# Kernel tuning notes

Hardware: AMD Instinct MI355X
Metric: run time of the kernel (lower is better)

The kernel has to match this reference:

```python
import jax, jax.numpy as jnp
import numpy as np

N_NODES = 50000
N_EDGES = 800000
C_IN = 128
C_OUT = 128


def setup_inputs() -> dict:
    key = jax.random.key(0)
    k1, k2, k3, k4 = jax.random.split(key, 4)
    x = jax.random.normal(k1, (N_NODES, C_IN), dtype=jnp.float32)
    edge_index = jax.random.randint(k2, (2, N_EDGES), 0, N_NODES, dtype=jnp.int64)
    # Linear(in, out): weight [out, in], bias [out]
    W = jax.random.normal(k3, (C_OUT, C_IN), dtype=jnp.float32) * (1.0 / np.sqrt(C_IN))
    b = jax.random.normal(k4, (C_OUT,), dtype=jnp.float32) * 0.01
    return {"x": x, "edge_index": edge_index, "W": W, "b": b}


def reference(x, edge_index, W, b):
    # GCN layer: out = D^{-1/2} (A + I) D^{-1/2} x W^T + b
    # Implemented as sparse gather/segment-sum (same math as the dense
    # adjacency matmul in the original, without the O(N^2) blowup).
    n = x.shape[0]
    loops = jnp.arange(n, dtype=edge_index.dtype)
    row = jnp.concatenate([edge_index[0], loops])  # [E+N]
    col = jnp.concatenate([edge_index[1], loops])  # [E+N]
    # degree over col index (as in pyg_utils.degree(edge_index[1], ...))
    ones = jnp.ones(row.shape[0], dtype=x.dtype)
    deg = jax.ops.segment_sum(ones, col, num_segments=n)
    deg_inv_sqrt = jnp.where(deg > 0, jax.lax.rsqrt(deg), 0.0).astype(x.dtype)
    norm = deg_inv_sqrt[row] * deg_inv_sqrt[col]  # [E+N]
    # aggregate: out[i] = sum_{(i,j) in edges} norm * x[j]
    msgs = x[col] * norm[:, None]  # [E+N, C_in]
    agg = jax.ops.segment_sum(msgs, row, num_segments=n)  # [N, C_in]
    return agg @ W.T + b
```

## Files before the change

### kernel.cpp

```cpp
#include <hip/hip_runtime.h>
#include <hip/hip_bf16.h>
#include <hip/hip_fp16.h>

#define C 128
#define NCH 32768
#define CN 2
#define CNODES (CN * NCH)
#define BE 64

typedef _Float16 f16x8 __attribute__((ext_vector_type(8)));
typedef _Float16 f16x4 __attribute__((ext_vector_type(4)));
typedef float f32x4 __attribute__((ext_vector_type(4)));

__global__ __launch_bounds__(256) void k_hist(
        const int* __restrict__ row, const int* __restrict__ col,
        unsigned char* __restrict__ part_row, unsigned char* __restrict__ part_col,
        unsigned char* __restrict__ tag, int E) {
    __shared__ unsigned lh[NCH / 4];
    int bid = blockIdx.x;
    int side = (bid >= CN * BE) ? 1 : 0;
    int lb = side ? bid - CN * BE : bid;
    int c = lb >> 6;
    int b = lb & (BE - 1);
    int tid = threadIdx.x;
    for (int i = tid * 4; i < NCH / 4; i += 1024) {
        lh[i] = 0u; lh[i + 1] = 0u; lh[i + 2] = 0u; lh[i + 3] = 0u;
    }
    __syncthreads();
    int EPB = (E + BE - 1) / BE;
    int base = b * EPB;
    int end = min(base + EPB, E);
    const int* src = side ? col : row;

#define PROC_ROW(rv, ev)                                                  \
    if (((unsigned)(rv) >> 15) == (unsigned)c) {                          \
        int loc = (rv) & (NCH - 1);                                       \
        unsigned sh = ((unsigned)loc & 3u) << 3;                          \
        unsigned old = atomicAdd(&lh[loc >> 2], 1u << sh);                \
        tag[ev] = (unsigned char)((old >> sh) & 0xffu);                   \
    }
#define PROC_COL(rv)                                                      \
    if (((unsigned)(rv) >> 15) == (unsigned)c) {                          \
        int loc = (rv) & (NCH - 1);                                       \
        atomicAdd(&lh[loc >> 2], 1u << (((unsigned)loc & 3u) << 3));      \
    }
    int nv = 0;
    if ((((uintptr_t)(src + base)) & 15) == 0) nv = (end - base) >> 2;
    const int4* src4 = (const int4*)(src + base);
    if (!side) {
        for (int it = tid; it < nv; it += 256) {
            int4 v = src4[it];
            int e0 = base + it * 4;
            PROC_ROW(v.x, e0);
            PROC_ROW(v.y, e0 + 1);
            PROC_ROW(v.z, e0 + 2);
            PROC_ROW(v.w, e0 + 3);
        }
        for (int e = base + nv * 4 + tid; e < end; e += 256) {
            int r = src[e];
            PROC_ROW(r, e);
        }
    } else {
        for (int it = tid; it < nv; it += 256) {
            int4 v = src4[it];
            PROC_COL(v.x);
            PROC_COL(v.y);
            PROC_COL(v.z);
            PROC_COL(v.w);
        }
        for (int e = base + nv * 4 + tid; e < end; e += 256) {
            int r = src[e];
            PROC_COL(r);
        }
    }
#undef PROC_ROW
#undef PROC_COL
    __syncthreads();
    unsigned* dst = (unsigned*)((side ? part_col : part_row) + (size_t)b * CNODES + c * NCH);
    for (int i = tid; i < NCH / 4; i += 256) dst[i] = lh[i];
}

__global__ __launch_bounds__(256) void k_reduce_scan(
        unsigned char* __restrict__ part_row, const unsigned char* __restrict__ part_col,
        unsigned* __restrict__ start, unsigned* __restrict__ bsum,
        float* __restrict__ dis, int n) {
    __shared__ unsigned s[256];
    int t = threadIdx.x;
    int i = blockIdx.x * 256 + t;
    unsigned acc = 0;
    if (i < n) {
#pragma unroll 8
        for (int b = 0; b < BE; ++b) {
            size_t off = (size_t)b * CNODES + i;
            unsigned v = part_row[off];
            part_row[off] = (unsigned char)acc;
            acc += v;
        }
        unsigned d = 0;
#pragma unroll 8
        for (int b = 0; b < BE; ++b) d += part_col[(size_t)b * CNODES + i];
        dis[i] = rsqrtf((float)(d + 1u));
    }
    unsigned v = acc;
    s[t] = v;
    __syncthreads();
    for (int off = 1; off < 256; off <<= 1) {
        unsigned add = (t >= off) ? s[t - off] : 0u;
        __syncthreads();
        s[t] += add;
        __syncthreads();
    }
    if (i < n) start[i] = s[t] - v;
    if (t == 255) bsum[blockIdx.x] = s[t];
}

__global__ __launch_bounds__(256) void k_scan_final(unsigned* __restrict__ start,
                                                    const unsigned* __restrict__ bsum,
                                                    int n, int E) {
    __shared__ unsigned s[256];
    int t = threadIdx.x;
    int bid = blockIdx.x;
    s[t] = (t < bid) ? bsum[t] : 0u;
    __syncthreads();
    for (int off = 128; off > 0; off >>= 1) {
        if (t < off) s[t] += s[t + off];
        __syncthreads();
    }
    unsigned base = s[0];
    int i = bid * 256 + t;
    if (i < n) start[i] += base;
    if (i == n) start[i] = (unsigned)E;
}

__global__ __launch_bounds__(256) void k_scatter_gemm(
        const int* __restrict__ row, const int* __restrict__ col,
        const unsigned char* __restrict__ tag, const unsigned char* __restrict__ boff,
        const unsigned* __restrict__ start, int* __restrict__ scol, int E, int SB,
        const float* __restrict__ A, const float* __restrict__ W,
        const float* __restrict__ dis, __half* __restrict__ Z16, int n) {
    __shared__ char lds[128 * 256];
    int bid = blockIdx.x;
    int tid = threadIdx.x;
    if (bid < SB) {
        int e = bid * 256 + tid;
        if (e < E) {
            int EPB = (E + BE - 1) / BE;
            unsigned b = (unsigned)e / (unsigned)EPB;
            int r = row[e];
            unsigned p = start[r] + boff[(size_t)b * CNODES + r] + tag[e];
            scol[p] = col[e];
        }
        return;
    }
    int w = tid >> 6, lane = tid & 63;
    int m0 = (bid - SB) * 128;

#pragma unroll
    for (int i = 0; i < 16; ++i) {
        int fidx = i * 256 + tid;
        int nr = fidx >> 5;
        int c4 = fidx & 31;
        float4 wv = *(const float4*)(W + (size_t)nr * C + c4 * 4);
        f16x4 hh = {(_Float16)wv.x, (_Float16)wv.y, (_Float16)wv.z, (_Float16)wv.w};
        unsigned byte = (unsigned)(nr * 256 + c4 * 8);
        byte ^= (unsigned)((nr & 7) << 4);
        *(f16x4*)(lds + byte) = hh;
    }
    __syncthreads();

    int rbase = m0 + w * 32;
    int q = lane >> 4, rl = lane & 15;
    float dm[2];
#pragma unroll
    for (int mt = 0; mt < 2; ++mt) {
        int r = rbase + mt * 16 + rl;
        dm[mt] = (r < n) ? dis[r] : 0.f;
    }
    f32x4 acc[2][8] = {};
#pragma unroll
    for (int kc = 0; kc < 4; ++kc) {
        f16x8 af[2];
#pragma unroll
        for (int mt = 0; mt < 2; ++mt) {
            int r = rbase + mt * 16 + rl;
            float4 x0 = make_float4(0.f, 0.f, 0.f, 0.f), x1 = x0;
            if (r < n) {
                const float* srcx = A + (size_t)r * C + kc * 32 + q * 8;
                x0 = *(const float4*)srcx;
                x1 = *(const float4*)(srcx + 4);
            }
            float s = dm[mt];
            af[mt][0] = (_Float16)(x0.x * s);
            af[mt][1] = (_Float16)(x0.y * s);
            af[mt][2] = (_Float16)(x0.z * s);
            af[mt][3] = (_Float16)(x0.w * s);
            af[mt][4] = (_Float16)(x1.x * s);
            af[mt][5] = (_Float16)(x1.y * s);
            af[mt][6] = (_Float16)(x1.z * s);
            af[mt][7] = (_Float16)(x1.w * s);
        }
#pragma unroll
        for (int nt = 0; nt < 8; ++nt) {
            int nrow = nt * 16 + rl;
            unsigned byte = (unsigned)(nrow * 256 + kc * 64 + q * 16);
            byte ^= (unsigned)((nrow & 7) << 4);
            f16x8 bf = *(f16x8*)(lds + byte);
            acc[0][nt] = __builtin_amdgcn_mfma_f32_16x16x32_f16(af[0], bf, acc[0][nt], 0, 0, 0);
            acc[1][nt] = __builtin_amdgcn_mfma_f32_16x16x32_f16(af[1], bf, acc[1][nt], 0, 0, 0);
        }
    }
    __syncthreads();

#pragma unroll
    for (int mt = 0; mt < 2; ++mt)
#pragma unroll
        for (int nt = 0; nt < 8; ++nt)
#pragma unroll
            for (int i = 0; i < 4; ++i) {
                int row_l = w * 32 + mt * 16 + q * 4 + i;
                int colh = nt * 16 + rl;
                unsigned byte = (unsigned)(row_l * 256 + colh * 2);
                byte ^= (unsigned)((row_l & 7) << 4);
                *(_Float16*)(lds + byte) = (_Float16)acc[mt][nt][i];
            }
    __syncthreads();

#pragma unroll
    for (int it = 0; it < 8; ++it) {
        int idx = it * 256 + tid;
        int row_l = idx >> 4, c8 = idx & 15;
        unsigned byte = (unsigned)(row_l * 256 + c8 * 16);
        byte ^= (unsigned)((row_l & 7) << 4);
        uint4 v = *(uint4*)(lds + byte);
        int gr = m0 + row_l;
        if (gr < n) *(uint4*)(Z16 + (size_t)gr * C + c8 * 8) = v;
    }
}

__device__ __forceinline__ void add8(uint4 v, float2& a0, float2& a1,
                                     float2& a2, float2& a3) {
    float2 f;
    f = __half22float2(*(__half2*)&v.x); a0.x += f.x; a0.y += f.y;
    f = __half22float2(*(__half2*)&v.y); a1.x += f.x; a1.y += f.y;
    f = __half22float2(*(__half2*)&v.z); a2.x += f.x; a2.y += f.y;
    f = __half22float2(*(__half2*)&v.w); a3.x += f.x; a3.y += f.y;
}

__global__ __launch_bounds__(256) void k_agg(const __half* __restrict__ Z16,
                                             const int* __restrict__ scol,
                                             const unsigned* __restrict__ start,
                                             const float* __restrict__ dis,
                                             const float* __restrict__ bias,
                                             float* __restrict__ out, int n) {
    int wid = threadIdx.x >> 6;
    int lane = threadIdx.x & 63;
    int slot = lane >> 4;
    int g = lane & 15;
    int r = blockIdx.x * 4 + wid;
    if (r >= n) return;
    unsigned s0 = start[r], s1 = start[r + 1];
    float dr = dis[r];
    const uint4* Z4 = (const uint4*)Z16;
    float2 a0 = {0.f, 0.f}, a1 = a0, a2 = a0, a3 = a0;
    if (slot == 0) {
        uint4 v = Z4[(size_t)r * 16 + g];
        add8(v, a0, a1, a2, a3);
    }
    unsigned k = s0;
    for (; k + 16 <= s1; k += 16) {
        int c0 = scol[k + slot];
        int c1 = scol[k + 4 + slot];
        int c2 = scol[k + 8 + slot];
        int c3 = scol[k + 12 + slot];
        uint4 v0 = Z4[(size_t)c0 * 16 + g];
        uint4 v1 = Z4[(size_t)c1 * 16 + g];
        uint4 v2 = Z4[(size_t)c2 * 16 + g];
        uint4 v3 = Z4[(size_t)c3 * 16 + g];
        add8(v0, a0, a1, a2, a3);
        add8(v1, a0, a1, a2, a3);
        add8(v2, a0, a1, a2, a3);
        add8(v3, a0, a1, a2, a3);
    }
    for (; k < s1; k += 4) {
        unsigned ke = k + slot;
        if (ke < s1) {
            int c = scol[ke];
            uint4 v = Z4[(size_t)c * 16 + g];
            add8(v, a0, a1, a2, a3);
        }
    }
    a0.x += __shfl_xor(a0.x, 16); a0.y += __shfl_xor(a0.y, 16);
    a1.x += __shfl_xor(a1.x, 16); a1.y += __shfl_xor(a1.y, 16);
    a2.x += __shfl_xor(a2.x, 16); a2.y += __shfl_xor(a2.y, 16);
    a3.x += __shfl_xor(a3.x, 16); a3.y += __shfl_xor(a3.y, 16);
    a0.x += __shfl_xor(a0.x, 32); a0.y += __shfl_xor(a0.y, 32);
    a1.x += __shfl_xor(a1.x, 32); a1.y += __shfl_xor(a1.y, 32);
    a2.x += __shfl_xor(a2.x, 32); a2.y += __shfl_xor(a2.y, 32);
    a3.x += __shfl_xor(a3.x, 32); a3.y += __shfl_xor(a3.y, 32);
    if (slot == 0) {
        float4 b0 = *(const float4*)(bias + g * 8);
        float4 b1 = *(const float4*)(bias + g * 8 + 4);
        float4 o0, o1;
        o0.x = b0.x + dr * a0.x; o0.y = b0.y + dr * a0.y;
        o0.z = b0.z + dr * a1.x; o0.w = b0.w + dr * a1.y;
        o1.x = b1.x + dr * a2.x; o1.y = b1.y + dr * a2.y;
        o1.z = b1.z + dr * a3.x; o1.w = b1.w + dr * a3.y;
        float* op = out + (size_t)r * C + g * 8;
        *(float4*)op = o0;
        *(float4*)(op + 4) = o1;
    }
}

extern "C" void kernel_launch(void* const* d_in, const int* in_sizes, int n_in,
                              void* d_out, int out_size, void* d_ws, size_t ws_size,
                              hipStream_t stream) {
    const float* x  = (const float*)d_in[0];
    const int*   ei = (const int*)d_in[1];
    const float* W  = (const float*)d_in[2];
    const float* b  = (const float*)d_in[3];
    float* out = (float*)d_out;

    int n = in_sizes[0] / C;
    int E = in_sizes[1] / 2;
    const int* row = ei;
    const int* col = ei + E;

    char* p = (char*)d_ws;
    size_t sz_part = (((size_t)BE * CNODES) + 511) & ~(size_t)511;
    size_t sz_n    = (((size_t)n * 4) + 511) & ~(size_t)511;
    size_t sz_n1   = (((size_t)(n + 1) * 4) + 511) & ~(size_t)511;
    size_t sz_E1   = (((size_t)E) + 511) & ~(size_t)511;
    size_t sz_E4   = (((size_t)E * 4) + 511) & ~(size_t)511;
    size_t off = 0;
    unsigned char*  part_row = (unsigned char*)(p + off);  off += sz_part;
    unsigned char*  part_col = (unsigned char*)(p + off);  off += sz_part;
    unsigned*       start    = (unsigned*)(p + off);       off += sz_n1;
    float*          dis      = (float*)(p + off);          off += sz_n;
    unsigned*       bsum     = (unsigned*)(p + off);       off += 4096;
    unsigned char*  tag      = (unsigned char*)(p + off);  off += sz_E1;
    int*            scol     = (int*)(p + off);            off += sz_E4;
    __half*         z16      = (__half*)(p + off);

    int NT = 256;
    int NB = (n + NT - 1) / NT;
    int SB = (E + NT - 1) / NT;
    int GB = (n + 127) / 128;

    k_hist<<<2 * CN * BE, NT, 0, stream>>>(row, col, part_row, part_col, tag, E);
    k_reduce_scan<<<NB, NT, 0, stream>>>(part_row, part_col, start, bsum, dis, n);
    k_scan_final<<<NB, NT, 0, stream>>>(start, bsum, n, E);
    k_scatter_gemm<<<SB + GB, NT, 0, stream>>>(row, col, tag, part_row, start, scol,
                                               E, SB, x, W, dis, z16, n);
    k_agg<<<(n + 3) / 4, NT, 0, stream>>>(z16, scol, start, dis, b, out, n);
}
```

Baseline: 81.23 us.

## Run GEMM alongside histogram kernel and apply degree scaling afterwards

The dense x·W^T GEMM moves out of the scatter kernel and into the histogram kernel, so it runs concurrently with the edge histogram. Because degrees are not known yet at that point, the D^{-1/2} row scaling is dropped from the GEMM and applied later in a separate elementwise pass over the fp16 result, fused into the scatter kernel. The edge-block count BE doubles to 128 and EPB is rounded to a multiple of 4 so the int4 loads stay aligned. The cost is an extra read and write of the fp16 Z matrix, plus an additional fp16 rounding step.

```diff
diff --git a/kernel.cpp b/kernel.cpp
--- a/kernel.cpp
+++ b/kernel.cpp
@@ -6,31 +6,36 @@
 #define NCH 32768
 #define CN 2
 #define CNODES (CN * NCH)
-#define BE 64
+#define BE 128
 
 typedef _Float16 f16x8 __attribute__((ext_vector_type(8)));
 typedef _Float16 f16x4 __attribute__((ext_vector_type(4)));
 typedef float f32x4 __attribute__((ext_vector_type(4)));
 
-__global__ __launch_bounds__(256) void k_hist(
+__global__ __launch_bounds__(256) void k_hist_gemm(
         const int* __restrict__ row, const int* __restrict__ col,
         unsigned char* __restrict__ part_row, unsigned char* __restrict__ part_col,
-        unsigned char* __restrict__ tag, int E) {
-    __shared__ unsigned lh[NCH / 4];
+        unsigned char* __restrict__ tag, int E, int EPB, int GB,
+        const float* __restrict__ A, const float* __restrict__ W,
+        __half* __restrict__ Y16, int n) {
+    __shared__ char lds[128 * 256];
     int bid = blockIdx.x;
-    int side = (bid >= CN * BE) ? 1 : 0;
-    int lb = side ? bid - CN * BE : bid;
-    int c = lb >> 6;
-    int b = lb & (BE - 1);
     int tid = threadIdx.x;
-    for (int i = tid * 4; i < NCH / 4; i += 1024) {
-        lh[i] = 0u; lh[i + 1] = 0u; lh[i + 2] = 0u; lh[i + 3] = 0u;
-    }
-    __syncthreads();
-    int EPB = (E + BE - 1) / BE;
-    int base = b * EPB;
-    int end = min(base + EPB, E);
-    const int* src = side ? col : row;
+
+    if (bid >= GB) {
+        unsigned* lh = (unsigned*)lds;
+        int lb = bid - GB;
+        int side = (lb >= CN * BE) ? 1 : 0;
+        if (side) lb -= CN * BE;
+        int c = lb >> 7;
+        int b = lb & (BE - 1);
+        for (int i = tid * 4; i < NCH / 4; i += 1024) {
+            lh[i] = 0u; lh[i + 1] = 0u; lh[i + 2] = 0u; lh[i + 3] = 0u;
+        }
+        __syncthreads();
+        int base = b * EPB;
+        int end = min(base + EPB, E);
+        const int* src = side ? col : row;
 
 #define PROC_ROW(rv, ev)                                                  \
     if (((unsigned)(rv) >> 15) == (unsigned)c) {                          \
@@ -44,40 +49,118 @@
         int loc = (rv) & (NCH - 1);                                       \
         atomicAdd(&lh[loc >> 2], 1u << (((unsigned)loc & 3u) << 3));      \
     }
-    int nv = 0;
-    if ((((uintptr_t)(src + base)) & 15) == 0) nv = (end - base) >> 2;
-    const int4* src4 = (const int4*)(src + base);
-    if (!side) {
-        for (int it = tid; it < nv; it += 256) {
-            int4 v = src4[it];
-            int e0 = base + it * 4;
-            PROC_ROW(v.x, e0);
-            PROC_ROW(v.y, e0 + 1);
-            PROC_ROW(v.z, e0 + 2);
-            PROC_ROW(v.w, e0 + 3);
-        }
-        for (int e = base + nv * 4 + tid; e < end; e += 256) {
-            int r = src[e];
-            PROC_ROW(r, e);
-        }
-    } else {
-        for (int it = tid; it < nv; it += 256) {
-            int4 v = src4[it];
-            PROC_COL(v.x);
-            PROC_COL(v.y);
-            PROC_COL(v.z);
-            PROC_COL(v.w);
-        }
-        for (int e = base + nv * 4 + tid; e < end; e += 256) {
-            int r = src[e];
-            PROC_COL(r);
-        }
-    }
+        int nv = (end > base) ? ((end - base) >> 2) : 0;
+        const int4* src4 = (const int4*)(src + base);
+        if (!side) {
+            for (int it = tid; it < nv; it += 256) {
+                int4 v = src4[it];
+                int e0 = base + it * 4;
+                PROC_ROW(v.x, e0);
+                PROC_ROW(v.y, e0 + 1);
+                PROC_ROW(v.z, e0 + 2);
+                PROC_ROW(v.w, e0 + 3);
+            }
+            for (int e = base + nv * 4 + tid; e < end; e += 256) {
+                int r = src[e];
+                PROC_ROW(r, e);
+            }
+        } else {
+            for (int it = tid; it < nv; it += 256) {
+                int4 v = src4[it];
+                PROC_COL(v.x);
+                PROC_COL(v.y);
+                PROC_COL(v.z);
+                PROC_COL(v.w);
+            }
+            for (int e = base + nv * 4 + tid; e < end; e += 256) {
+                int r = src[e];
+                PROC_COL(r);
+            }
+        }
 #undef PROC_ROW
 #undef PROC_COL
-    __syncthreads();
-    unsigned* dst = (unsigned*)((side ? part_col : part_row) + (size_t)b * CNODES + c * NCH);
-    for (int i = tid; i < NCH / 4; i += 256) dst[i] = lh[i];
+        __syncthreads();
+        unsigned* dst = (unsigned*)((side ? part_col : part_row) + (size_t)b * CNODES + c * NCH);
+        for (int i = tid; i < NCH / 4; i += 256) dst[i] = lh[i];
+        return;
+    }
+
+    int w = tid >> 6, lane = tid & 63;
+    int m0 = bid * 128;
+
+#pragma unroll
+    for (int i = 0; i < 16; ++i) {
+        int fidx = i * 256 + tid;
+        int nr = fidx >> 5;
+        int c4 = fidx & 31;
+        float4 wv = *(const float4*)(W + (size_t)nr * C + c4 * 4);
+        f16x4 hh = {(_Float16)wv.x, (_Float16)wv.y, (_Float16)wv.z, (_Float16)wv.w};
+        unsigned byte = (unsigned)(nr * 256 + c4 * 8);
+        byte ^= (unsigned)((nr & 7) << 4);
+        *(f16x4*)(lds + byte) = hh;
+    }
+    __syncthreads();
+
+    int rbase = m0 + w * 32;
+    int q = lane >> 4, rl = lane & 15;
+    f32x4 acc[2][8] = {};
+#pragma unroll
+    for (int kc = 0; kc < 4; ++kc) {
+        f16x8 af[2];
+#pragma unroll
+        for (int mt = 0; mt < 2; ++mt) {
+            int r = rbase + mt * 16 + rl;
+            float4 x0 = make_float4(0.f, 0.f, 0.f, 0.f), x1 = x0;
+            if (r < n) {
+                const float* srcx = A + (size_t)r * C + kc * 32 + q * 8;
+                x0 = *(const float4*)srcx;
+                x1 = *(const float4*)(srcx + 4);
+            }
+            af[mt][0] = (_Float16)x0.x;
+            af[mt][1] = (_Float16)x0.y;
+            af[mt][2] = (_Float16)x0.z;
+            af[mt][3] = (_Float16)x0.w;
+            af[mt][4] = (_Float16)x1.x;
+            af[mt][5] = (_Float16)x1.y;
+            af[mt][6] = (_Float16)x1.z;
+            af[mt][7] = (_Float16)x1.w;
+        }
+#pragma unroll
+        for (int nt = 0; nt < 8; ++nt) {
+            int nrow = nt * 16 + rl;
+            unsigned byte = (unsigned)(nrow * 256 + kc * 64 + q * 16);
+            byte ^= (unsigned)((nrow & 7) << 4);
+            f16x8 bf = *(f16x8*)(lds + byte);
+            acc[0][nt] = __builtin_amdgcn_mfma_f32_16x16x32_f16(af[0], bf, acc[0][nt], 0, 0, 0);
+            acc[1][nt] = __builtin_amdgcn_mfma_f32_16x16x32_f16(af[1], bf, acc[1][nt], 0, 0, 0);
+        }
+    }
+    __syncthreads();
+
+#pragma unroll
+    for (int mt = 0; mt < 2; ++mt)
+#pragma unroll
+        for (int nt = 0; nt < 8; ++nt)
+#pragma unroll
+            for (int i = 0; i < 4; ++i) {
+                int row_l = w * 32 + mt * 16 + q * 4 + i;
+                int colh = nt * 16 + rl;
+                unsigned byte = (unsigned)(row_l * 256 + colh * 2);
+                byte ^= (unsigned)((row_l & 7) << 4);
+                *(_Float16*)(lds + byte) = (_Float16)acc[mt][nt][i];
+            }
+    __syncthreads();
+
+#pragma unroll
+    for (int it = 0; it < 8; ++it) {
+        int idx = it * 256 + tid;
+        int row_l = idx >> 4, c8 = idx & 15;
+        unsigned byte = (unsigned)(row_l * 256 + c8 * 16);
+        byte ^= (unsigned)((row_l & 7) << 4);
+        uint4 v = *(uint4*)(lds + byte);
+        int gr = m0 + row_l;
+        if (gr < n) *(uint4*)(Y16 + (size_t)gr * C + c8 * 8) = v;
+    }
 }
 
 __global__ __launch_bounds__(256) void k_reduce_scan(
@@ -132,19 +215,17 @@
     if (i == n) start[i] = (unsigned)E;
 }
 
-__global__ __launch_bounds__(256) void k_scatter_gemm(
+__global__ __launch_bounds__(256) void k_scatter_scale(
         const int* __restrict__ row, const int* __restrict__ col,
         const unsigned char* __restrict__ tag, const unsigned char* __restrict__ boff,
-        const unsigned* __restrict__ start, int* __restrict__ scol, int E, int SB,
-        const float* __restrict__ A, const float* __restrict__ W,
-        const float* __restrict__ dis, __half* __restrict__ Z16, int n) {
-    __shared__ char lds[128 * 256];
+        const unsigned* __restrict__ start, int* __restrict__ scol,
+        int E, int EPB, int SB,
+        __half* __restrict__ Z16, const float* __restrict__ dis, int n) {
     int bid = blockIdx.x;
     int tid = threadIdx.x;
     if (bid < SB) {
         int e = bid * 256 + tid;
         if (e < E) {
-            int EPB = (E + BE - 1) / BE;
             unsigned b = (unsigned)e / (unsigned)EPB;
             int r = row[e];
             unsigned p = start[r] + boff[(size_t)b * CNODES + r] + tag[e];
@@ -152,88 +233,19 @@
         }
         return;
     }
-    int w = tid >> 6, lane = tid & 63;
-    int m0 = (bid - SB) * 128;
-
-#pragma unroll
-    for (int i = 0; i < 16; ++i) {
-        int fidx = i * 256 + tid;
-        int nr = fidx >> 5;
-        int c4 = fidx & 31;
-        float4 wv = *(const float4*)(W + (size_t)nr * C + c4 * 4);
-        f16x4 hh = {(_Float16)wv.x, (_Float16)wv.y, (_Float16)wv.z, (_Float16)wv.w};
-        unsigned byte = (unsigned)(nr * 256 + c4 * 8);
-        byte ^= (unsigned)((nr & 7) << 4);
-        *(f16x4*)(lds + byte) = hh;
-    }
-    __syncthreads();
-
-    int rbase = m0 + w * 32;
-    int q = lane >> 4, rl = lane & 15;
-    float dm[2];
-#pragma unroll
-    for (int mt = 0; mt < 2; ++mt) {
-        int r = rbase + mt * 16 + rl;
-        dm[mt] = (r < n) ? dis[r] : 0.f;
-    }
-    f32x4 acc[2][8] = {};
-#pragma unroll
-    for (int kc = 0; kc < 4; ++kc) {
-        f16x8 af[2];
-#pragma unroll
-        for (int mt = 0; mt < 2; ++mt) {
-            int r = rbase + mt * 16 + rl;
-            float4 x0 = make_float4(0.f, 0.f, 0.f, 0.f), x1 = x0;
-            if (r < n) {
-                const float* srcx = A + (size_t)r * C + kc * 32 + q * 8;
-                x0 = *(const float4*)srcx;
-                x1 = *(const float4*)(srcx + 4);
-            }
-            float s = dm[mt];
-            af[mt][0] = (_Float16)(x0.x * s);
-            af[mt][1] = (_Float16)(x0.y * s);
-            af[mt][2] = (_Float16)(x0.z * s);
-            af[mt][3] = (_Float16)(x0.w * s);
-            af[mt][4] = (_Float16)(x1.x * s);
-            af[mt][5] = (_Float16)(x1.y * s);
-            af[mt][6] = (_Float16)(x1.z * s);
-            af[mt][7] = (_Float16)(x1.w * s);
-        }
-#pragma unroll
-        for (int nt = 0; nt < 8; ++nt) {
-            int nrow = nt * 16 + rl;
-            unsigned byte = (unsigned)(nrow * 256 + kc * 64 + q * 16);
-            byte ^= (unsigned)((nrow & 7) << 4);
-            f16x8 bf = *(f16x8*)(lds + byte);
-            acc[0][nt] = __builtin_amdgcn_mfma_f32_16x16x32_f16(af[0], bf, acc[0][nt], 0, 0, 0);
-            acc[1][nt] = __builtin_amdgcn_mfma_f32_16x16x32_f16(af[1], bf, acc[1][nt], 0, 0, 0);
-        }
-    }
-    __syncthreads();
-
-#pragma unroll
-    for (int mt = 0; mt < 2; ++mt)
-#pragma unroll
-        for (int nt = 0; nt < 8; ++nt)
-#pragma unroll
-            for (int i = 0; i < 4; ++i) {
-                int row_l = w * 32 + mt * 16 + q * 4 + i;
-                int colh = nt * 16 + rl;
-                unsigned byte = (unsigned)(row_l * 256 + colh * 2);
-                byte ^= (unsigned)((row_l & 7) << 4);
-                *(_Float16*)(lds + byte) = (_Float16)acc[mt][nt][i];
-            }
-    __syncthreads();
-
-#pragma unroll
-    for (int it = 0; it < 8; ++it) {
-        int idx = it * 256 + tid;
-        int row_l = idx >> 4, c8 = idx & 15;
-        unsigned byte = (unsigned)(row_l * 256 + c8 * 16);
-        byte ^= (unsigned)((row_l & 7) << 4);
-        uint4 v = *(uint4*)(lds + byte);
-        int gr = m0 + row_l;
-        if (gr < n) *(uint4*)(Z16 + (size_t)gr * C + c8 * 8) = v;
+    int idx = (bid - SB) * 256 + tid;
+    if (idx < n * 16) {
+        int r = idx >> 4;
+        float dr = dis[r];
+        uint4* Z4 = (uint4*)Z16;
+        uint4 v = Z4[idx];
+        __half2* hp = (__half2*)&v;
+#pragma unroll
+        for (int j = 0; j < 4; ++j) {
+            float2 f = __half22float2(hp[j]);
+            hp[j] = __floats2half2_rn(f.x * dr, f.y * dr);
+        }
+        Z4[idx] = v;
     }
 }
 
@@ -343,13 +355,16 @@
 
     int NT = 256;
     int NB = (n + NT - 1) / NT;
+    int EPB = (((E + BE - 1) / BE) + 3) & ~3;
     int SB = (E + NT - 1) / NT;
+    int ZB = (n * 16 + NT - 1) / NT;
     int GB = (n + 127) / 128;
 
-    k_hist<<<2 * CN * BE, NT, 0, stream>>>(row, col, part_row, part_col, tag, E);
+    k_hist_gemm<<<GB + 2 * CN * BE, NT, 0, stream>>>(row, col, part_row, part_col,
+                                                     tag, E, EPB, GB, x, W, z16, n);
     k_reduce_scan<<<NB, NT, 0, stream>>>(part_row, part_col, start, bsum, dis, n);
     k_scan_final<<<NB, NT, 0, stream>>>(start, bsum, n, E);
-    k_scatter_gemm<<<SB + GB, NT, 0, stream>>>(row, col, tag, part_row, start, scol,
-                                               E, SB, x, W, dis, z16, n);
+    k_scatter_scale<<<SB + ZB, NT, 0, stream>>>(row, col, tag, part_row, start, scol,
+                                                E, EPB, SB, z16, dis, n);
     k_agg<<<(n + 3) / 4, NT, 0, stream>>>(z16, scol, start, dis, b, out, n);
 }
```

Result: slower. 88.00 us (+8.3%).

## Pad CSR segments to multiples of 16 with dummy zero row to drop tail loop

Applied to the files above, without the earlier changes.

Each node's neighbour list is rounded up to a multiple of 16 in the scan, and the column array is prefilled with index n, which points to an extra zero row appended to Z16. The aggregation kernel then runs only the 16-wide unrolled loop and no longer needs the divergent per-slot tail loop. In exchange it loads more padding rows (average degree is about 16, so padding adds roughly half again as many gathers), writes a larger scol fill in the histogram kernel, and uses more workspace.

```diff
diff --git a/kernel.cpp b/kernel.cpp
--- a/kernel.cpp
+++ b/kernel.cpp
@@ -15,14 +15,27 @@
 __global__ __launch_bounds__(256) void k_hist(
         const int* __restrict__ row, const int* __restrict__ col,
         unsigned char* __restrict__ part_row, unsigned char* __restrict__ part_col,
-        unsigned char* __restrict__ tag, int E) {
+        unsigned char* __restrict__ tag, int E,
+        int* __restrict__ scol, int cap4, __half* __restrict__ Z16, int n) {
     __shared__ unsigned lh[NCH / 4];
     int bid = blockIdx.x;
+    int tid = threadIdx.x;
+    if (bid >= 2 * CN * BE) {
+        int fb = bid - 2 * CN * BE;
+        int idx = fb * 256 + tid;
+        if (idx < cap4) {
+            int4 nv = make_int4(n, n, n, n);
+            ((int4*)scol)[idx] = nv;
+        }
+        if (fb == 0 && tid < 16) {
+            ((uint4*)(Z16 + (size_t)n * C))[tid] = make_uint4(0u, 0u, 0u, 0u);
+        }
+        return;
+    }
     int side = (bid >= CN * BE) ? 1 : 0;
     int lb = side ? bid - CN * BE : bid;
     int c = lb >> 6;
     int b = lb & (BE - 1);
-    int tid = threadIdx.x;
     for (int i = tid * 4; i < NCH / 4; i += 1024) {
         lh[i] = 0u; lh[i + 1] = 0u; lh[i + 2] = 0u; lh[i + 3] = 0u;
     }
@@ -101,7 +114,7 @@
         for (int b = 0; b < BE; ++b) d += part_col[(size_t)b * CNODES + i];
         dis[i] = rsqrtf((float)(d + 1u));
     }
-    unsigned v = acc;
+    unsigned v = (i < n) ? ((acc + 15u) & ~15u) : 0u;
     s[t] = v;
     __syncthreads();
     for (int off = 1; off < 256; off <<= 1) {
@@ -110,13 +123,13 @@
         s[t] += add;
         __syncthreads();
     }
-    if (i < n) start[i] = s[t] - v;
+    if (i <= n) start[i] = s[t] - v;
     if (t == 255) bsum[blockIdx.x] = s[t];
 }
 
 __global__ __launch_bounds__(256) void k_scan_final(unsigned* __restrict__ start,
                                                     const unsigned* __restrict__ bsum,
-                                                    int n, int E) {
+                                                    int n) {
     __shared__ unsigned s[256];
     int t = threadIdx.x;
     int bid = blockIdx.x;
@@ -128,8 +141,7 @@
     }
     unsigned base = s[0];
     int i = bid * 256 + t;
-    if (i < n) start[i] += base;
-    if (i == n) start[i] = (unsigned)E;
+    if (i <= n) start[i] += base;
 }
 
 __global__ __launch_bounds__(256) void k_scatter_gemm(
@@ -266,8 +278,7 @@
         uint4 v = Z4[(size_t)r * 16 + g];
         add8(v, a0, a1, a2, a3);
     }
-    unsigned k = s0;
-    for (; k + 16 <= s1; k += 16) {
+    for (unsigned k = s0; k < s1; k += 16) {
         int c0 = scol[k + slot];
         int c1 = scol[k + 4 + slot];
         int c2 = scol[k + 8 + slot];
@@ -280,14 +291,6 @@
         add8(v1, a0, a1, a2, a3);
         add8(v2, a0, a1, a2, a3);
         add8(v3, a0, a1, a2, a3);
-    }
-    for (; k < s1; k += 4) {
-        unsigned ke = k + slot;
-        if (ke < s1) {
-            int c = scol[ke];
-            uint4 v = Z4[(size_t)c * 16 + g];
-            add8(v, a0, a1, a2, a3);
-        }
     }
     a0.x += __shfl_xor(a0.x, 16); a0.y += __shfl_xor(a0.y, 16);
     a1.x += __shfl_xor(a1.x, 16); a1.y += __shfl_xor(a1.y, 16);
@@ -326,11 +329,12 @@
     const int* col = ei + E;
 
     char* p = (char*)d_ws;
+    size_t cap  = (size_t)E + 15 * (size_t)n;
     size_t sz_part = (((size_t)BE * CNODES) + 511) & ~(size_t)511;
     size_t sz_n    = (((size_t)n * 4) + 511) & ~(size_t)511;
     size_t sz_n1   = (((size_t)(n + 1) * 4) + 511) & ~(size_t)511;
     size_t sz_E1   = (((size_t)E) + 511) & ~(size_t)511;
-    size_t sz_E4   = (((size_t)E * 4) + 511) & ~(size_t)511;
+    size_t sz_cap  = ((cap * 4) + 511) & ~(size_t)511;
     size_t off = 0;
     unsigned char*  part_row = (unsigned char*)(p + off);  off += sz_part;
     unsigned char*  part_col = (unsigned char*)(p + off);  off += sz_part;
@@ -338,17 +342,20 @@
     float*          dis      = (float*)(p + off);          off += sz_n;
     unsigned*       bsum     = (unsigned*)(p + off);       off += 4096;
     unsigned char*  tag      = (unsigned char*)(p + off);  off += sz_E1;
-    int*            scol     = (int*)(p + off);            off += sz_E4;
+    int*            scol     = (int*)(p + off);            off += sz_cap;
     __half*         z16      = (__half*)(p + off);
 
     int NT = 256;
     int NB = (n + NT - 1) / NT;
     int SB = (E + NT - 1) / NT;
     int GB = (n + 127) / 128;
-
-    k_hist<<<2 * CN * BE, NT, 0, stream>>>(row, col, part_row, part_col, tag, E);
+    int cap4 = (int)((cap + 3) / 4);
+    int FB = (cap4 + NT - 1) / NT;
+
+    k_hist<<<2 * CN * BE + FB, NT, 0, stream>>>(row, col, part_row, part_col, tag, E,
+                                                scol, cap4, z16, n);
     k_reduce_scan<<<NB, NT, 0, stream>>>(part_row, part_col, start, bsum, dis, n);
-    k_scan_final<<<NB, NT, 0, stream>>>(start, bsum, n, E);
+    k_scan_final<<<NB, NT, 0, stream>>>(start, bsum, n);
     k_scatter_gemm<<<SB + GB, NT, 0, stream>>>(row, col, tag, part_row, start, scol,
                                                E, SB, x, W, dis, z16, n);
     k_agg<<<(n + 3) / 4, NT, 0, stream>>>(z16, scol, start, dis, b, out, n);
```

Result: faster. 79.05 us (-2.7%).
